# Kernel tuning notes

Hardware: AMD Instinct MI355X
Metric: run time of the kernel (lower is better)

Reference implementation:

```python
import jax, jax.numpy as jnp
import numpy as np

ALPHA = 0.2  # LeakyReLU negative slope


def setup_inputs() -> dict:
    key = jax.random.key(0)
    k1, k2, k3, k4 = jax.random.split(key, 4)
    bs, L, D, F_in, F_out = 8, 4096, 16, 128, 128
    x = jax.random.normal(k1, (bs, L, F_in), dtype=jnp.float32)
    adj = jax.random.randint(k2, (bs, L, D), 0, L, dtype=jnp.int64)
    # xavier_normal-ish init for params
    W = jax.random.normal(k3, (F_in, F_out), dtype=jnp.float32) * (1.414 * (2.0 / (F_in + F_out)) ** 0.5)
    a = jax.random.normal(k4, (2 * F_out, 1), dtype=jnp.float32) * (1.414 * (2.0 / (2 * F_out + 1)) ** 0.5)
    return {"x": x, "adj": adj, "W": W, "a": a}


def reference(x, adj, W, a):
    # x: [B, L, F_in], adj: [B, L, D] int node indices, W: [F_in, F_out], a: [2*F_out, 1]
    # Project first, then gather (same math as gather-then-project, fewer FLOPs).
    h = jnp.matmul(x, W)                                  # [B, L, F_out]
    h_prime = jax.vmap(lambda hb, ab: hb[ab])(h, adj)     # [B, L, D, F_out]
    # h_node: neighbor-0 features broadcast over D (torch repeat_interleave of h_prime[:,:,0:1,:])
    h_node = jnp.broadcast_to(h_prime[:, :, :1, :], h_prime.shape)
    # attention logits: concat(h_prime, h_node) @ a -> [B, L, D, 1]
    e = jnp.concatenate([h_prime, h_node], axis=-1) @ a
    e = jnp.where(e > 0, e, ALPHA * e)                    # LeakyReLU
    attn = jax.nn.softmax(e[..., 0], axis=-1)             # softmax over neighbors D -> [B, L, D]
    # dropout is identity in eval mode (p=0.0)
    out = jnp.einsum('bld,bldf->blf', attn, h_prime)      # weighted aggregate -> [B, L, F_out]
    return jax.nn.elu(out)                                # concat=True branch
```

## Files before the change

kernel.cpp:

```cpp
#include <hip/hip_runtime.h>
#include <hip/hip_bf16.h>

#define BATCH 8
#define SEQ   4096
#define DEG   16
#define FD    128
#define NTOT  (BATCH * SEQ)
#define ALPHA 0.2f
#define LDS_WK 132

typedef __attribute__((ext_vector_type(8))) short short8v;
typedef __attribute__((ext_vector_type(4))) short short4v;
typedef __attribute__((ext_vector_type(4))) float float4v;
typedef __attribute__((ext_vector_type(4))) float f32x4;
typedef __attribute__((ext_vector_type(2))) float f32x2;

__device__ __forceinline__ unsigned short f2bf(float f) {
    unsigned int u = __float_as_uint(f);
    u += 0x7fffu + ((u >> 16) & 1u);
    return (unsigned short)(u >> 16);
}

__global__ __launch_bounds__(256) void gat_proj(
    const float* __restrict__ x, const float* __restrict__ W,
    const float* __restrict__ avec, unsigned short* __restrict__ hb,
    float2* __restrict__ s12)
{
    __shared__ unsigned short Wt[128 * LDS_WK];

    const int t = threadIdx.x;
    const int bid = blockIdx.x;
    const int xcd = bid & 7, blk = bid >> 3;
    const long long rowBase = (long long)xcd * SEQ + (long long)blk * 64;

    {
        const int q = t & 31;
        const int kh = t >> 5;
        #pragma unroll
        for (int j = 0; j < 8; ++j) {
            const int kp = kh + 8 * j;
            const f32x4 w0 = *reinterpret_cast<const f32x4*>(&W[(2 * kp) * FD + 4 * q]);
            const f32x4 w1 = *reinterpret_cast<const f32x4*>(&W[(2 * kp + 1) * FD + 4 * q]);
            #pragma unroll
            for (int e2 = 0; e2 < 4; ++e2) {
                const unsigned int pk = (unsigned int)f2bf(w0[e2])
                                      | ((unsigned int)f2bf(w1[e2]) << 16);
                *reinterpret_cast<unsigned int*>(&Wt[(4 * q + e2) * LDS_WK + 2 * kp]) = pk;
            }
        }
    }

    const int lane = t & 63, wv = t >> 6;
    const int g = lane >> 4, mrow = lane & 15;
    const long long node = rowBase + wv * 16 + mrow;
    short8v xfrag[4];
    {
        const float* xr = x + node * FD + 4 * g;
        #pragma unroll
        for (int kb = 0; kb < 4; ++kb) {
            const f32x4 x0 = __builtin_nontemporal_load(
                reinterpret_cast<const f32x4*>(xr + 32 * kb));
            const f32x4 x1 = __builtin_nontemporal_load(
                reinterpret_cast<const f32x4*>(xr + 32 * kb + 16));
            short8v f;
            f[0] = (short)f2bf(x0[0]); f[1] = (short)f2bf(x0[1]);
            f[2] = (short)f2bf(x0[2]); f[3] = (short)f2bf(x0[3]);
            f[4] = (short)f2bf(x1[0]); f[5] = (short)f2bf(x1[1]);
            f[6] = (short)f2bf(x1[2]); f[7] = (short)f2bf(x1[3]);
            xfrag[kb] = f;
        }
    }
    __syncthreads();

    float4v acc[8];
    #pragma unroll
    for (int tn = 0; tn < 8; ++tn) { acc[tn][0] = 0.f; acc[tn][1] = 0.f; acc[tn][2] = 0.f; acc[tn][3] = 0.f; }

    #pragma unroll
    for (int tn = 0; tn < 8; ++tn) {
        const int nbase = (16 * tn + mrow) * LDS_WK + 4 * g;
        #pragma unroll
        for (int kb = 0; kb < 4; ++kb) {
            const short4v lo = *reinterpret_cast<const short4v*>(&Wt[nbase + 32 * kb]);
            const short4v hi = *reinterpret_cast<const short4v*>(&Wt[nbase + 32 * kb + 16]);
            short8v wf;
            wf[0] = lo[0]; wf[1] = lo[1]; wf[2] = lo[2]; wf[3] = lo[3];
            wf[4] = hi[0]; wf[5] = hi[1]; wf[6] = hi[2]; wf[7] = hi[3];
            acc[tn] = __builtin_amdgcn_mfma_f32_16x16x32_bf16(wf, xfrag[kb], acc[tn], 0, 0, 0);
        }
    }

    float s1p = 0.f, s2p = 0.f;
    #pragma unroll
    for (int tn = 0; tn < 8; ++tn) {
        const int col = 16 * tn + 4 * g;
        const unsigned int u0 = (unsigned int)f2bf(acc[tn][0])
                              | ((unsigned int)f2bf(acc[tn][1]) << 16);
        const unsigned int u1 = (unsigned int)f2bf(acc[tn][2])
                              | ((unsigned int)f2bf(acc[tn][3]) << 16);
        *reinterpret_cast<uint2*>(&hb[node * FD + col]) = make_uint2(u0, u1);
        const f32x4 a1 = *reinterpret_cast<const f32x4*>(&avec[col]);
        const f32x4 a2 = *reinterpret_cast<const f32x4*>(&avec[FD + col]);
        #pragma unroll
        for (int r = 0; r < 4; ++r) {
            s1p = fmaf(acc[tn][r], a1[r], s1p);
            s2p = fmaf(acc[tn][r], a2[r], s2p);
        }
    }
    s1p += __shfl_xor(s1p, 16, 64);  s2p += __shfl_xor(s2p, 16, 64);
    s1p += __shfl_xor(s1p, 32, 64);  s2p += __shfl_xor(s2p, 32, 64);
    if (lane < 16)
        s12[rowBase + wv * 16 + lane] = make_float2(s1p, s2p);
}

__global__ __launch_bounds__(256) void gat_aggr(
    const int* __restrict__ adj, const unsigned short* __restrict__ hb,
    const float2* __restrict__ s12, float* __restrict__ out)
{
    const int t = threadIdx.x;
    const int lane = t & 63;
    const int wv_u = __builtin_amdgcn_readfirstlane(t) >> 6;
    const int bid = blockIdx.x;
    const int xcd = bid & 7, blk = bid >> 3;
    const int bBase = xcd * SEQ;
    const int nodeLoc0 = blk * 16 + wv_u * 4;

    const int a_l = adj[((long long)(bBase + nodeLoc0)) * DEG + lane];

    const float2 sv = s12[bBase + a_l];
    const float s2n0 = __shfl(sv.y, lane & 48, 64);
    float ev = sv.x + s2n0;
    ev = ev > 0.f ? ev : ALPHA * ev;
    float p = __expf(ev);
    float sum = p;
    #pragma unroll
    for (int mo = 1; mo < 16; mo <<= 1) sum += __shfl_xor(sum, mo, 64);
    p *= 1.f / sum;

    #pragma unroll
    for (int j = 0; j < 4; ++j) {
        const long long node = (long long)bBase + nodeLoc0 + j;
        float a0 = 0.f, a1 = 0.f;
        #pragma unroll
        for (int d = 0; d < 16; ++d) {
            const int nbjd = __builtin_amdgcn_readlane(a_l, 16 * j + d);
            const float pd = __uint_as_float(
                __builtin_amdgcn_readlane(__float_as_uint(p), 16 * j + d));
            const unsigned int* rp = reinterpret_cast<const unsigned int*>(
                hb + (((long long)(bBase + nbjd)) << 7));
            const unsigned int u = rp[lane];
            a0 = fmaf(pd, __uint_as_float(u << 16), a0);
            a1 = fmaf(pd, __uint_as_float(u & 0xffff0000u), a1);
        }
        f32x2 o;
        o[0] = a0 > 0.f ? a0 : (__expf(a0) - 1.f);
        o[1] = a1 > 0.f ? a1 : (__expf(a1) - 1.f);
        __builtin_nontemporal_store(o, reinterpret_cast<f32x2*>(
            out + node * FD + lane * 2));
    }
}

extern "C" void kernel_launch(void* const* d_in, const int* in_sizes, int n_in,
                              void* d_out, int out_size, void* d_ws, size_t ws_size,
                              hipStream_t stream) {
    const float* x  = (const float*)d_in[0];
    const int* adj  = (const int*)d_in[1];
    const float* W  = (const float*)d_in[2];
    const float* a  = (const float*)d_in[3];
    float* out = (float*)d_out;

    unsigned short* hb = (unsigned short*)d_ws;
    float2* s12 = (float2*)((char*)d_ws + (size_t)NTOT * FD * 2);

    gat_proj<<<dim3(NTOT / 64), dim3(256), 0, stream>>>(x, W, a, hb, s12);
    gat_aggr<<<dim3(NTOT / 16), dim3(256), 0, stream>>>(adj, hb, s12, out);
}
```

Before: 22.90 us.

## Split projection output columns across two waves per row tile with 512-thread blocks

The projection kernel now uses 512 threads per block. Each pair of waves shares a 16-row tile and splits the 128 output columns in half, so each wave does half the MFMAs and holds half the accumulators. The partial attention dot products are combined through shared memory with an extra barrier, and the W staging loop is reindexed for more threads. The x loads also change from nontemporal to normal loads. This raises wave-level parallelism and lowers register pressure, but each x fragment is loaded twice, once per wave in the pair.

```diff
diff --git a/kernel.cpp b/kernel.cpp
--- a/kernel.cpp
+++ b/kernel.cpp
@@ -21,12 +21,13 @@
     return (unsigned short)(u >> 16);
 }
 
-__global__ __launch_bounds__(256) void gat_proj(
+__global__ __launch_bounds__(512, 4) void gat_proj(
     const float* __restrict__ x, const float* __restrict__ W,
     const float* __restrict__ avec, unsigned short* __restrict__ hb,
     float2* __restrict__ s12)
 {
     __shared__ unsigned short Wt[128 * LDS_WK];
+    __shared__ float2 sbuf[4][16];
 
     const int t = threadIdx.x;
     const int bid = blockIdx.x;
@@ -34,11 +35,11 @@
     const long long rowBase = (long long)xcd * SEQ + (long long)blk * 64;
 
     {
-        const int q = t & 31;
-        const int kh = t >> 5;
+        const int q = t >> 4;
+        const int kp0 = t & 15;
         #pragma unroll
-        for (int j = 0; j < 8; ++j) {
-            const int kp = kh + 8 * j;
+        for (int j = 0; j < 4; ++j) {
+            const int kp = kp0 + 16 * j;
             const f32x4 w0 = *reinterpret_cast<const f32x4*>(&W[(2 * kp) * FD + 4 * q]);
             const f32x4 w1 = *reinterpret_cast<const f32x4*>(&W[(2 * kp + 1) * FD + 4 * q]);
             #pragma unroll
@@ -51,17 +52,16 @@
     }
 
     const int lane = t & 63, wv = t >> 6;
+    const int wr = wv >> 1, wc = wv & 1;
     const int g = lane >> 4, mrow = lane & 15;
-    const long long node = rowBase + wv * 16 + mrow;
+    const long long node = rowBase + wr * 16 + mrow;
     short8v xfrag[4];
     {
         const float* xr = x + node * FD + 4 * g;
         #pragma unroll
         for (int kb = 0; kb < 4; ++kb) {
-            const f32x4 x0 = __builtin_nontemporal_load(
-                reinterpret_cast<const f32x4*>(xr + 32 * kb));
-            const f32x4 x1 = __builtin_nontemporal_load(
-                reinterpret_cast<const f32x4*>(xr + 32 * kb + 16));
+            const f32x4 x0 = *reinterpret_cast<const f32x4*>(xr + 32 * kb);
+            const f32x4 x1 = *reinterpret_cast<const f32x4*>(xr + 32 * kb + 16);
             short8v f;
             f[0] = (short)f2bf(x0[0]); f[1] = (short)f2bf(x0[1]);
             f[2] = (short)f2bf(x0[2]); f[3] = (short)f2bf(x0[3]);
@@ -72,12 +72,13 @@
     }
     __syncthreads();
 
-    float4v acc[8];
+    float4v acc[4];
     #pragma unroll
-    for (int tn = 0; tn < 8; ++tn) { acc[tn][0] = 0.f; acc[tn][1] = 0.f; acc[tn][2] = 0.f; acc[tn][3] = 0.f; }
+    for (int tn = 0; tn < 4; ++tn) { acc[tn][0] = 0.f; acc[tn][1] = 0.f; acc[tn][2] = 0.f; acc[tn][3] = 0.f; }
 
     #pragma unroll
-    for (int tn = 0; tn < 8; ++tn) {
+    for (int tp = 0; tp < 4; ++tp) {
+        const int tn = 4 * wc + tp;
         const int nbase = (16 * tn + mrow) * LDS_WK + 4 * g;
         #pragma unroll
         for (int kb = 0; kb < 4; ++kb) {
@@ -86,31 +87,35 @@
             short8v wf;
             wf[0] = lo[0]; wf[1] = lo[1]; wf[2] = lo[2]; wf[3] = lo[3];
             wf[4] = hi[0]; wf[5] = hi[1]; wf[6] = hi[2]; wf[7] = hi[3];
-            acc[tn] = __builtin_amdgcn_mfma_f32_16x16x32_bf16(wf, xfrag[kb], acc[tn], 0, 0, 0);
+            acc[tp] = __builtin_amdgcn_mfma_f32_16x16x32_bf16(wf, xfrag[kb], acc[tp], 0, 0, 0);
         }
     }
 
     float s1p = 0.f, s2p = 0.f;
     #pragma unroll
-    for (int tn = 0; tn < 8; ++tn) {
-        const int col = 16 * tn + 4 * g;
-        const unsigned int u0 = (unsigned int)f2bf(acc[tn][0])
-                              | ((unsigned int)f2bf(acc[tn][1]) << 16);
-        const unsigned int u1 = (unsigned int)f2bf(acc[tn][2])
-                              | ((unsigned int)f2bf(acc[tn][3]) << 16);
+    for (int tp = 0; tp < 4; ++tp) {
+        const int col = 16 * (4 * wc + tp) + 4 * g;
+        const unsigned int u0 = (unsigned int)f2bf(acc[tp][0])
+                              | ((unsigned int)f2bf(acc[tp][1]) << 16);
+        const unsigned int u1 = (unsigned int)f2bf(acc[tp][2])
+                              | ((unsigned int)f2bf(acc[tp][3]) << 16);
         *reinterpret_cast<uint2*>(&hb[node * FD + col]) = make_uint2(u0, u1);
         const f32x4 a1 = *reinterpret_cast<const f32x4*>(&avec[col]);
         const f32x4 a2 = *reinterpret_cast<const f32x4*>(&avec[FD + col]);
         #pragma unroll
         for (int r = 0; r < 4; ++r) {
-            s1p = fmaf(acc[tn][r], a1[r], s1p);
-            s2p = fmaf(acc[tn][r], a2[r], s2p);
+            s1p = fmaf(acc[tp][r], a1[r], s1p);
+            s2p = fmaf(acc[tp][r], a2[r], s2p);
         }
     }
     s1p += __shfl_xor(s1p, 16, 64);  s2p += __shfl_xor(s2p, 16, 64);
     s1p += __shfl_xor(s1p, 32, 64);  s2p += __shfl_xor(s2p, 32, 64);
-    if (lane < 16)
-        s12[rowBase + wv * 16 + lane] = make_float2(s1p, s2p);
+    if (wc == 1 && lane < 16) sbuf[wr][lane] = make_float2(s1p, s2p);
+    __syncthreads();
+    if (wc == 0 && lane < 16) {
+        const float2 o = sbuf[wr][lane];
+        s12[rowBase + wr * 16 + lane] = make_float2(s1p + o.x, s2p + o.y);
+    }
 }
 
 __global__ __launch_bounds__(256) void gat_aggr(
@@ -172,6 +177,6 @@
     unsigned short* hb = (unsigned short*)d_ws;
     float2* s12 = (float2*)((char*)d_ws + (size_t)NTOT * FD * 2);
 
-    gat_proj<<<dim3(NTOT / 64), dim3(256), 0, stream>>>(x, W, a, hb, s12);
+    gat_proj<<<dim3(NTOT / 64), dim3(512), 0, stream>>>(x, W, a, hb, s12);
     gat_aggr<<<dim3(NTOT / 16), dim3(256), 0, stream>>>(adj, hb, s12, out);
 }
```

Result: slower. 25.56 us (+11.6%).
